# Kernel optimization log

Measured on AMD Instinct MI355X. Metric: run time of the kernel, lower is better.

Reference implementation:

```python
import jax, jax.numpy as jnp
import numpy as np

IH, IW = 32, 32
HEADS, DIM_HEAD = 8, 32
EPS = 1e-6


def conv3x3(x, w):
    # x: [B,C,H,W], w: [O,I,3,3], stride 1, pad 1, no bias
    return jax.lax.conv_general_dilated(x, w, (1, 1), ((1, 1), (1, 1)),
                                        dimension_numbers=('NCHW', 'OIHW', 'NCHW'))


def groupnorm1(x, g, b):
    # GroupNorm(1, C): normalize over (C,H,W) per sample
    mu = jnp.mean(x, axis=(1, 2, 3), keepdims=True)
    var = jnp.var(x, axis=(1, 2, 3), keepdims=True)
    xn = (x - mu) * jax.lax.rsqrt(var + EPS)
    return xn * g[None, :, None, None] + b[None, :, None, None]


def proj(x, w, g, b):
    return jax.nn.gelu(groupnorm1(conv3x3(x, w), g, b), approximate=False)


def relative_index(ih, iw):
    coords = np.stack(np.meshgrid(np.arange(ih), np.arange(iw), indexing='ij')).reshape(2, -1)
    rel = coords[:, :, None] - coords[:, None, :]  # [2, n, n]
    rel[0] += ih - 1
    rel[1] += iw - 1
    rel[0] *= 2 * iw - 1
    return jnp.asarray(rel.sum(0).reshape(-1))  # [n*n]


def setup_inputs() -> dict:
    key = jax.random.key(0)
    ks = jax.random.split(key, 9)
    C = HEADS * DIM_HEAD  # 256
    B = 8
    s = 0.02
    inp = {
        'x': jax.random.normal(ks[0], (B, C, IH, IW), jnp.float32),
        'wq': jax.random.normal(ks[1], (C, C, 3, 3), jnp.float32) * s,
        'wk': jax.random.normal(ks[2], (C, C, 3, 3), jnp.float32) * s,
        'wv': jax.random.normal(ks[3], (C, C, 3, 3), jnp.float32) * s,
        'gq': jnp.ones((C,), jnp.float32), 'bq': jnp.zeros((C,), jnp.float32),
        'gk': jnp.ones((C,), jnp.float32), 'bk': jnp.zeros((C,), jnp.float32),
        'gv': jnp.ones((C,), jnp.float32), 'bv': jnp.zeros((C,), jnp.float32),
        'bias_table': jax.random.normal(ks[4], ((2 * IH - 1) * (2 * IW - 1), HEADS), jnp.float32) * s,
        'wo': jax.random.normal(ks[5], (C, C), jnp.float32) * s,
        'bo': jnp.zeros((C,), jnp.float32),
    }
    return inp


def reference(x, wq, wk, wv, gq, bq, gk, bk, gv, bv, bias_table, wo, bo):
    B, C, ih, iw = x.shape
    n = ih * iw
    h, d = HEADS, DIM_HEAD

    q = proj(x, wq, gq, bq)  # [B,C,H,W]
    k = proj(x, wk, gk, bk)
    v = proj(x, wv, gv, bv)

    # 'b c ih iw -> b (ih iw) c' then 'b n (h d) -> b h n d'  ==  [B,h,d,n] -> [B,h,n,d]
    def to_heads(t):
        return t.reshape(B, h, d, n).transpose(0, 1, 3, 2)

    q4, k4, v4 = to_heads(q), to_heads(k), to_heads(v)

    # NOTE: original code applies self.scale only when y is not None; y=None here -> no scale.
    dots = jnp.einsum('bhnd,bhmd->bhnm', q4, k4)  # [B,h,n,n]

    rel_idx = relative_index(ih, iw)  # [n*n]
    rel_bias = bias_table[rel_idx].reshape(n, n, h).transpose(2, 0, 1)[None]  # [1,h,n,n]

    attn = jax.nn.softmax(dots + rel_bias, axis=-1)
    out = jnp.einsum('bhnm,bhmd->bhnd', attn, v4)  # [B,h,n,d]

    # 'b h n d -> b n (h d)' then 'b (ih iw) c -> b c ih iw'
    out = out.transpose(0, 2, 1, 3).reshape(B, n, C).transpose(0, 2, 1).reshape(B, C, ih, iw)

    # to_out: 1x1 conv with bias (dropout=0 in eval)
    out = jnp.einsum('oc,bchw->bohw', wo, out) + bo[None, :, None, None]
    return out
```

## Files before the change

kernel.cpp:

```cpp
#include <hip/hip_runtime.h>
#include <cstdint>
#include <cstddef>

#define GEPS 1e-6f

using bf16x8 = __attribute__((ext_vector_type(8))) short;
using f32x4  = __attribute__((ext_vector_type(4))) float;

__device__ inline ushort f2bf(float x) {
    union { float f; uint32_t u; } v; v.f = x;
    uint32_t r = (v.u + 0x7fffu + ((v.u >> 16) & 1u)) >> 16;
    return (ushort)r;
}
__device__ inline float bf2f(ushort b) {
    union { float f; uint32_t u; } v; v.u = ((uint32_t)b) << 16;
    return v.f;
}

__device__ inline void gll16(const void* g, void* l) {
    __builtin_amdgcn_global_load_lds(
        (const __attribute__((address_space(1))) void*)g,
        (__attribute__((address_space(3))) void*)l, 16, 0, 0);
}

__global__ __launch_bounds__(256) void prep_k(
    const float* __restrict__ x,
    const float* __restrict__ wq, const float* __restrict__ wk,
    const float* __restrict__ wv, const float* __restrict__ wo,
    const float* __restrict__ btab,
    ushort* __restrict__ Xcl, ushort* __restrict__ Wbuf,
    ushort* __restrict__ wo_bf, ushort* __restrict__ Bx,
    float* __restrict__ stats)
{
    __shared__ __align__(16) ushort Xs[3 * 34 * 128];
    int tid = threadIdx.x;
    int blk = blockIdx.x;

    if (blk < 256) {
        int b = blk >> 5, y = blk & 31;
#pragma unroll
        for (int it = 0; it < 8; ++it) {
            int idx = it * 256 + tid;
            int ci = idx >> 3, pxg = idx & 7;
            float4 v = *(const float4*)&x[((size_t)(b * 256 + ci)) * 1024 + y * 32 + pxg * 4];
            int base = (pxg * 4) * 264 + ci;
            Xs[base + 0 * 264] = f2bf(v.x);
            Xs[base + 1 * 264] = f2bf(v.y);
            Xs[base + 2 * 264] = f2bf(v.z);
            Xs[base + 3 * 264] = f2bf(v.w);
        }
        __syncthreads();
        uint4 z4 = make_uint4(0u, 0u, 0u, 0u);
        ushort* orow = Xcl + ((size_t)(b * 34) + y + 1) * 34 * 256;
#pragma unroll
        for (int it = 0; it < 4; ++it) {
            int idx = it * 256 + tid;
            int px = idx >> 5, ci8 = idx & 31;
            *(uint4*)&orow[(px + 1) * 256 + ci8 * 8] =
                *(const uint4*)&Xs[px * 264 + ci8 * 8];
        }
        if (tid < 64) {
            int side = tid >> 5, ci8 = tid & 31;
            *(uint4*)&orow[side * 33 * 256 + ci8 * 8] = z4;
        }
        if (y == 0 || y == 31) {
            ushort* zrow = Xcl + ((size_t)(b * 34) + (y == 0 ? 0 : 33)) * 34 * 256;
#pragma unroll
            for (int it = 0; it < 5; ++it) {
                int idx = it * 256 + tid;
                if (idx < 1088) *(uint4*)&zrow[idx * 8] = z4;
            }
        }
        return;
    }
    if (blk < 1024) {
        int wrow = blk - 256;
        int proj = wrow >> 8, co = wrow & 255;
        const float* src = ((proj == 0) ? wq : ((proj == 1) ? wk : wv)) + (size_t)co * 2304;
#pragma unroll
        for (int j = 0; j < 9; ++j) {
            int idx = j * 256 + tid;
            Xs[idx] = f2bf(src[idx]);
        }
        __syncthreads();
        ushort* dst = Wbuf + (size_t)wrow * 2304;
#pragma unroll
        for (int j = 0; j < 9; ++j)
            dst[j * 256 + tid] = Xs[tid * 9 + j];
        return;
    }
    if (blk < 1088) {
        if (blk == 1024 && tid < 192) stats[tid] = 0.f;
        int t = (blk - 1024) * 256 + tid;
        float4 v = *(const float4*)&wo[(size_t)t * 4];
        union { uint2 u; ushort s[4]; } o;
        o.s[0] = f2bf(v.x); o.s[1] = f2bf(v.y); o.s[2] = f2bf(v.z); o.s[3] = f2bf(v.w);
        *(uint2*)&wo_bf[(size_t)t * 4] = o.u;
        return;
    }
    int g = (blk - 1088) * 4 + (tid >> 6);
    int l = tid & 63;
    int h = g >> 10, qt = (g >> 4) & 63, kt = g & 15;
    int quad = l >> 4, c = l & 15;
    union { uint4 v[2]; ushort s[16]; } o;
#pragma unroll
    for (int f = 0; f < 4; ++f)
#pragma unroll
        for (int r = 0; r < 4; ++r) {
            int qrow = qt * 16 + quad * 4 + r;
            int key = kt * 64 + f * 16 + c;
            int dy = (qrow >> 5) - (key >> 5) + 31;
            int dx = (qrow & 31) - (key & 31) + 31;
            o.s[f * 4 + r] = f2bf(btab[(dy * 63 + dx) * 8 + h]);
        }
    uint4* dst = (uint4*)(Bx + ((size_t)g * 64 + l) * 16);
    dst[0] = o.v[0];
    dst[1] = o.v[1];
}

__global__ __launch_bounds__(256, 3) void gemm_bt(
    const ushort* __restrict__ A, const ushort* __restrict__ B,
    int M, int N, int K,
    ushort* __restrict__ Cpart, float* __restrict__ stats,
    float* __restrict__ Cout, const float* __restrict__ bias, int mode)
{
    __shared__ __align__(16) ushort As[128 * 64];
    __shared__ __align__(16) ushort Bs[64 * 64];
    __shared__ float red[8];
    int tid = threadIdx.x;
    int mbase = blockIdx.x * 128, nbase = blockIdx.y * 64;
    int wave = tid >> 6, lane = tid & 63;
    int wm = wave & 1, wn = wave >> 1;
    int quad = lane >> 4, c = lane & 15;

    int row_s = tid >> 3;
    int cc8 = (tid & 7) ^ (row_s & 7);
    ushort* ldsA = As + wave * 512;
    ushort* ldsB = Bs + wave * 512;

    int rb[4];
    if (mode == 0) {
#pragma unroll
        for (int R = 0; R < 4; ++R) {
            int r = mbase + R * 32 + row_s;
            int b_ = r >> 10, yy = (r >> 5) & 31, xx = r & 31;
            rb[R] = ((b_ * 34 + yy) * 34 + xx) * 256;
        }
    }

    f32x4 acc[4][2];
#pragma unroll
    for (int i = 0; i < 4; ++i)
#pragma unroll
        for (int j = 0; j < 2; ++j) acc[i][j] = (f32x4){0.f, 0.f, 0.f, 0.f};

    for (int kb = 0; kb < K; kb += 64) {
        __syncthreads();
        if (mode == 0) {
            int tap = kb >> 8;
            int kh = (tap * 11) >> 5;
            int kw = tap - kh * 3;
            int toff = (kh * 34 + kw) * 256 + (kb & 255) + cc8 * 8;
#pragma unroll
            for (int R = 0; R < 4; ++R)
                gll16(A + rb[R] + toff, ldsA + R * 2048);
#pragma unroll
            for (int S = 0; S < 2; ++S)
                gll16(B + (size_t)(nbase + S * 32 + row_s) * K + kb + cc8 * 8,
                      ldsB + S * 2048);
        } else {
#pragma unroll
            for (int R = 0; R < 4; ++R)
                gll16(A + (size_t)(mbase + R * 32 + row_s) * K + kb + cc8 * 8,
                      ldsA + R * 2048);
#pragma unroll
            for (int S = 0; S < 2; ++S)
                gll16(B + (size_t)(nbase + S * 32 + row_s) * K + kb + cc8 * 8,
                      ldsB + S * 2048);
        }
        __syncthreads();
#pragma unroll
        for (int kq = 0; kq < 2; ++kq) {
            bf16x8 af[4], bfr[2];
            int sw = ((kq * 4 + quad) ^ (c & 7)) * 8;
#pragma unroll
            for (int i = 0; i < 4; ++i)
                af[i]  = *(const bf16x8*)&As[(wm * 64 + i * 16 + c) * 64 + sw];
#pragma unroll
            for (int j = 0; j < 2; ++j)
                bfr[j] = *(const bf16x8*)&Bs[(wn * 32 + j * 16 + c) * 64 + sw];
#pragma unroll
            for (int i = 0; i < 4; ++i)
#pragma unroll
                for (int j = 0; j < 2; ++j)
                    acc[i][j] = __builtin_amdgcn_mfma_f32_16x16x32_bf16(
                        af[i], bfr[j], acc[i][j], 0, 0, 0);
        }
    }

    if (mode == 0) {
        float s1 = 0.f, s2 = 0.f;
#pragma unroll
        for (int i = 0; i < 4; ++i) {
            int mrow = mbase + wm * 64 + i * 16 + quad * 4;
#pragma unroll
            for (int j = 0; j < 2; ++j) {
                int ncol = nbase + wn * 32 + j * 16 + c;
#pragma unroll
                for (int r = 0; r < 4; ++r) {
                    float v = acc[i][j][r];
                    s1 += v; s2 += v * v;
                    Cpart[(size_t)(mrow + r) * N + ncol] = f2bf(v);
                }
            }
        }
#pragma unroll
        for (int mk = 1; mk < 64; mk <<= 1) {
            s1 += __shfl_xor(s1, mk, 64);
            s2 += __shfl_xor(s2, mk, 64);
        }
        if (lane == 0) { red[wave] = s1; red[4 + wave] = s2; }
        __syncthreads();
        if (tid == 0) {
            int key = (blockIdx.y >> 2) * 8 + (blockIdx.x >> 3);
            atomicAdd(&stats[key * 2 + 0], red[0] + red[1] + red[2] + red[3]);
            atomicAdd(&stats[key * 2 + 1], red[4] + red[5] + red[6] + red[7]);
        }
    } else {
#pragma unroll
        for (int i = 0; i < 4; ++i) {
            int mrow0 = mbase + wm * 64 + i * 16 + quad * 4;
#pragma unroll
            for (int j = 0; j < 2; ++j) {
                int ncol = nbase + wn * 32 + j * 16 + c;
                int bb = ncol >> 10, px = ncol & 1023;
#pragma unroll
                for (int r = 0; r < 4; ++r) {
                    int o = mrow0 + r;
                    Cout[((size_t)bb * 256 + o) * 1024 + px] = acc[i][j][r] + bias[o];
                }
            }
        }
    }
}

__global__ void gn_k(const ushort* __restrict__ P0,
                     const float* __restrict__ stats,
                     const float* __restrict__ gq, const float* __restrict__ bq,
                     const float* __restrict__ gk, const float* __restrict__ bk,
                     const float* __restrict__ gv, const float* __restrict__ bv,
                     ushort* __restrict__ qb, ushort* __restrict__ kb2,
                     ushort* __restrict__ vx)
{
    int t = blockIdx.x * 256 + threadIdx.x;
    int m = t / 96;
    int nn = (t - m * 96) * 8;
    int proj = nn >> 8, co = nn & 255;
    int b = m >> 10, px = m & 1023;
    float s1 = stats[(proj * 8 + b) * 2 + 0];
    float s2 = stats[(proj * 8 + b) * 2 + 1];
    const float Ninv = 1.f / 262144.f;
    float mu = s1 * Ninv;
    float var = fmaxf(s2 * Ninv - mu * mu, 0.f);
    float rsig = rsqrtf(var + GEPS);
    const float* gam = (proj == 0) ? gq : ((proj == 1) ? gk : gv);
    const float* bet = (proj == 0) ? bq : ((proj == 1) ? bk : bv);

    size_t base = (size_t)m * 768 + nn;
    union { uint4 v; ushort s[8]; } a;
    a.v = *(const uint4*)&P0[base];
    union { uint4 v; ushort s[8]; } outp;
#pragma unroll
    for (int e = 0; e < 8; ++e) {
        int cc = co + e;
        float xv = bf2f(a.s[e]);
        float xn = (xv - mu) * rsig * gam[cc] + bet[cc];
        float ge = 0.5f * xn * (1.f + erff(xn * 0.70710678118654752f));
        outp.s[e] = f2bf(ge);
    }
    int h = co >> 5, d = co & 31;
    if (proj == 0) {
        *(uint4*)(qb + ((((size_t)b * 8 + h) * 1024 + px) * 32 + d)) = outp.v;
    } else if (proj == 1) {
        *(uint4*)(kb2 + ((((size_t)b * 8 + h) * 1024 + px) * 32 + d)) = outp.v;
    } else {
        ushort* vb = vx + ((size_t)b * 8 + h) * 32768;
        int kca = px >> 5, quad = (px >> 3) & 3, j = px & 7;
#pragma unroll
        for (int e = 0; e < 8; ++e) {
            int dd = d + e;
            vb[(((kca * 2 + (dd >> 4)) * 64) + quad * 16 + (dd & 15)) * 8 + j] = outp.s[e];
        }
    }
}

__global__ __launch_bounds__(256, 8) void attn_k(
    const ushort* __restrict__ qb, const ushort* __restrict__ kb,
    const ushort* __restrict__ vx, const ushort* __restrict__ Bx,
    ushort* __restrict__ attnout)
{
    __shared__ __align__(16) ushort Pl[4 * 16 * 72];
    int tid = threadIdx.x, wave = tid >> 6, lane = tid & 63;
    int quad = lane >> 4, c = lane & 15;
    int bh = blockIdx.y;
    int h = bh & 7;
    int qbase = blockIdx.x * 64 + wave * 16;

    const ushort* Q  = qb + (size_t)bh * 1024 * 32;
    const ushort* Kp = kb + (size_t)bh * 1024 * 32;
    const ushort* Vb = vx + (size_t)bh * 32768;
    const ushort* bxp = Bx + (((size_t)(h * 64 + (qbase >> 4)) * 16) * 64 + lane) * 16;
    ushort* Pw = Pl + wave * 16 * 72;

    bf16x8 qf = *(const bf16x8*)&Q[(qbase + c) * 32 + quad * 8];

    float l_[4] = {0.f, 0.f, 0.f, 0.f};
    f32x4 Of0 = {0.f, 0.f, 0.f, 0.f}, Of1 = {0.f, 0.f, 0.f, 0.f};

    for (int kb64 = 0; kb64 < 1024; kb64 += 64) {
        f32x4 S[4];
        f32x4 zf = {0.f, 0.f, 0.f, 0.f};
#pragma unroll
        for (int f = 0; f < 4; ++f) {
            bf16x8 kf = *(const bf16x8*)&Kp[(kb64 + f * 16 + c) * 32 + quad * 8];
            S[f] = __builtin_amdgcn_mfma_f32_16x16x32_bf16(qf, kf, zf, 0, 0, 0);
        }
        union { uint4 v[2]; ushort s[16]; } bu;
        const uint4* bsrc = (const uint4*)(bxp + (size_t)(kb64 >> 6) * 1024);
        bu.v[0] = bsrc[0];
        bu.v[1] = bsrc[1];
#pragma unroll
        for (int f = 0; f < 4; ++f)
#pragma unroll
            for (int r = 0; r < 4; ++r) {
                float p = __expf(S[f][r] + bf2f(bu.s[f * 4 + r]));
                S[f][r] = p;
                l_[r] += p;
            }
#pragma unroll
        for (int f = 0; f < 4; ++f)
#pragma unroll
            for (int r = 0; r < 4; ++r)
                Pw[(quad * 4 + r) * 72 + f * 16 + c] = f2bf(S[f][r]);
#pragma unroll
        for (int kc = 0; kc < 2; ++kc) {
            int kca = (kb64 >> 5) + kc;
            bf16x8 pf = *(const bf16x8*)&Pw[c * 72 + kc * 32 + quad * 8];
            bf16x8 vf0 = *(const bf16x8*)&Vb[((kca * 2 + 0) * 64 + lane) * 8];
            Of0 = __builtin_amdgcn_mfma_f32_16x16x32_bf16(pf, vf0, Of0, 0, 0, 0);
            bf16x8 vf1 = *(const bf16x8*)&Vb[((kca * 2 + 1) * 64 + lane) * 8];
            Of1 = __builtin_amdgcn_mfma_f32_16x16x32_bf16(pf, vf1, Of1, 0, 0, 0);
        }
    }
    int b = bh >> 3;
#pragma unroll
    for (int r = 0; r < 4; ++r) {
        float l = l_[r];
        l += __shfl_xor(l, 1, 64);
        l += __shfl_xor(l, 2, 64);
        l += __shfl_xor(l, 4, 64);
        l += __shfl_xor(l, 8, 64);
        float inv = 1.f / l;
        int qr = qbase + quad * 4 + r;
        ushort* dst = attnout + ((size_t)b * 1024 + qr) * 256 + h * 32;
        dst[c]      = f2bf(Of0[r] * inv);
        dst[16 + c] = f2bf(Of1[r] * inv);
    }
}

extern "C" void kernel_launch(void* const* d_in, const int* in_sizes, int n_in,
                              void* d_out, int out_size, void* d_ws, size_t ws_size,
                              hipStream_t stream)
{
    const float* x    = (const float*)d_in[0];
    const float* wq   = (const float*)d_in[1];
    const float* wk   = (const float*)d_in[2];
    const float* wv   = (const float*)d_in[3];
    const float* gq   = (const float*)d_in[4];
    const float* bq   = (const float*)d_in[5];
    const float* gk   = (const float*)d_in[6];
    const float* bk   = (const float*)d_in[7];
    const float* gv   = (const float*)d_in[8];
    const float* bv   = (const float*)d_in[9];
    const float* btab = (const float*)d_in[10];
    const float* wo   = (const float*)d_in[11];
    const float* bo   = (const float*)d_in[12];
    float* out = (float*)d_out;

    char* w = (char*)d_ws;
    size_t off = 0;
    auto alloc = [&](size_t bytes) -> char* {
        char* p = w + off;
        off += (bytes + 255) & ~(size_t)255;
        return p;
    };
    ushort* Xcl     = (ushort*)alloc(8ull * 34 * 34 * 256 * 2);
    ushort* Wbuf    = (ushort*)alloc(768ull * 2304 * 2);
    ushort* wo_bf   = (ushort*)alloc(65536ull * 2);
    ushort* Bx      = (ushort*)alloc(8192ull * 64 * 16 * 2);
    ushort* P0      = (ushort*)alloc(8192ull * 768 * 2);
    float*  stats   = (float*)alloc(768);
    ushort* qb      = (ushort*)alloc(8ull * 8 * 1024 * 32 * 2);
    ushort* kb2     = (ushort*)alloc(8ull * 8 * 1024 * 32 * 2);
    ushort* vx      = (ushort*)alloc(8ull * 8 * 32 * 1024 * 2);
    ushort* attnout = (ushort*)alloc(8ull * 1024 * 256 * 2);

    prep_k<<<3136, 256, 0, stream>>>(x, wq, wk, wv, wo, btab,
                                     Xcl, Wbuf, wo_bf, Bx, stats);
    gemm_bt<<<dim3(64, 12, 1), 256, 0, stream>>>(Xcl, Wbuf, 8192, 768, 2304,
                                                 P0, stats, nullptr, nullptr, 0);
    gn_k<<<3072, 256, 0, stream>>>(P0, stats, gq, bq, gk, bk, gv, bv,
                                   qb, kb2, vx);
    attn_k<<<dim3(16, 64, 1), 256, 0, stream>>>(qb, kb2, vx, Bx, attnout);
    gemm_bt<<<dim3(2, 128, 1), 256, 0, stream>>>(wo_bf, attnout, 256, 8192, 256,
                                                 nullptr, nullptr, out, bo, 1);
}
```

Before: 230.2 us.

## Split attention over two key halves and combine partial results

The attention kernel now splits the key dimension into two halves across a new grid z-dimension, doubling the block count. Each half writes unnormalized bf16 partial outputs and row sums, and a new combine kernel adds them and normalizes. This targets underutilization from the long serial key loop with only 1024 blocks, at the cost of an extra launch, extra global traffic, and rounding partial outputs to bf16 before summing.

```diff
diff --git a/kernel.cpp b/kernel.cpp
--- a/kernel.cpp
+++ b/kernel.cpp
@@ -297,13 +297,14 @@
 __global__ __launch_bounds__(256, 8) void attn_k(
     const ushort* __restrict__ qb, const ushort* __restrict__ kb,
     const ushort* __restrict__ vx, const ushort* __restrict__ Bx,
-    ushort* __restrict__ attnout)
+    ushort* __restrict__ Opart, float* __restrict__ lpart)
 {
     __shared__ __align__(16) ushort Pl[4 * 16 * 72];
     int tid = threadIdx.x, wave = tid >> 6, lane = tid & 63;
     int quad = lane >> 4, c = lane & 15;
     int bh = blockIdx.y;
     int h = bh & 7;
+    int z = blockIdx.z;
     int qbase = blockIdx.x * 64 + wave * 16;
 
     const ushort* Q  = qb + (size_t)bh * 1024 * 32;
@@ -317,7 +318,7 @@
     float l_[4] = {0.f, 0.f, 0.f, 0.f};
     f32x4 Of0 = {0.f, 0.f, 0.f, 0.f}, Of1 = {0.f, 0.f, 0.f, 0.f};
 
-    for (int kb64 = 0; kb64 < 1024; kb64 += 64) {
+    for (int kb64 = z * 512; kb64 < z * 512 + 512; kb64 += 64) {
         f32x4 S[4];
         f32x4 zf = {0.f, 0.f, 0.f, 0.f};
 #pragma unroll
@@ -352,7 +353,6 @@
             Of1 = __builtin_amdgcn_mfma_f32_16x16x32_bf16(pf, vf1, Of1, 0, 0, 0);
         }
     }
-    int b = bh >> 3;
 #pragma unroll
     for (int r = 0; r < 4; ++r) {
         float l = l_[r];
@@ -360,12 +360,33 @@
         l += __shfl_xor(l, 2, 64);
         l += __shfl_xor(l, 4, 64);
         l += __shfl_xor(l, 8, 64);
-        float inv = 1.f / l;
         int qr = qbase + quad * 4 + r;
-        ushort* dst = attnout + ((size_t)b * 1024 + qr) * 256 + h * 32;
-        dst[c]      = f2bf(Of0[r] * inv);
-        dst[16 + c] = f2bf(Of1[r] * inv);
-    }
+        size_t ob = (((size_t)z * 64 + bh) * 1024 + qr) * 32;
+        Opart[ob + c]      = f2bf(Of0[r]);
+        Opart[ob + 16 + c] = f2bf(Of1[r]);
+        if (c == 0) lpart[(size_t)z * 65536 + bh * 1024 + qr] = l;
+    }
+}
+
+__global__ __launch_bounds__(256) void combine_k(const ushort* __restrict__ Opart,
+                                                 const float* __restrict__ lpart,
+                                                 ushort* __restrict__ attnout)
+{
+    int t = blockIdx.x * 256 + threadIdx.x;
+    int g = t & 3;
+    int qg = t >> 2;
+    int bh = qg >> 10, qr = qg & 1023;
+    int b = bh >> 3, h = bh & 7;
+    size_t ob = ((size_t)qg) * 32 + g * 8;
+    union { uint4 v; ushort s[8]; } o0, o1;
+    o0.v = *(const uint4*)&Opart[ob];
+    o1.v = *(const uint4*)&Opart[(size_t)64 * 1024 * 32 + ob];
+    float inv = 1.f / (lpart[qg] + lpart[65536 + qg]);
+    union { uint4 u; ushort s[8]; } o;
+#pragma unroll
+    for (int e = 0; e < 8; ++e)
+        o.s[e] = f2bf((bf2f(o0.s[e]) + bf2f(o1.s[e])) * inv);
+    *(uint4*)&attnout[(((size_t)b * 1024 + qr) * 256) + h * 32 + g * 8] = o.u;
 }
 
 extern "C" void kernel_launch(void* const* d_in, const int* in_sizes, int n_in,
@@ -400,6 +421,8 @@
     ushort* Bx      = (ushort*)alloc(8192ull * 64 * 16 * 2);
     ushort* P0      = (ushort*)alloc(8192ull * 768 * 2);
     float*  stats   = (float*)alloc(768);
+    ushort* Opart   = (ushort*)alloc(2ull * 64 * 1024 * 32 * 2);
+    float*  lpart   = (float*)alloc(2ull * 64 * 1024 * 4);
     ushort* qb      = (ushort*)alloc(8ull * 8 * 1024 * 32 * 2);
     ushort* kb2     = (ushort*)alloc(8ull * 8 * 1024 * 32 * 2);
     ushort* vx      = (ushort*)alloc(8ull * 8 * 32 * 1024 * 2);
@@ -411,7 +434,8 @@
                                                  P0, stats, nullptr, nullptr, 0);
     gn_k<<<3072, 256, 0, stream>>>(P0, stats, gq, bq, gk, bk, gv, bv,
                                    qb, kb2, vx);
-    attn_k<<<dim3(16, 64, 1), 256, 0, stream>>>(qb, kb2, vx, Bx, attnout);
+    attn_k<<<dim3(16, 64, 2), 256, 0, stream>>>(qb, kb2, vx, Bx, Opart, lpart);
+    combine_k<<<1024, 256, 0, stream>>>(Opart, lpart, attnout);
     gemm_bt<<<dim3(2, 128, 1), 256, 0, stream>>>(wo_bf, attnout, 256, 8192, 256,
                                                  nullptr, nullptr, out, bo, 1);
 }
```

Measured after the change: 221.2 us. 1.04x faster.
